# Kernel optimization log

Hardware: AMD Instinct MI355X
Metric: run time of the kernel (lower is better)

Reference implementation:

```python
import jax, jax.numpy as jnp
import numpy as np

B, C, H, W = 8, 256, 64, 64
CQK = C // 8


def setup_inputs() -> dict:
    key = jax.random.key(0)
    ks = jax.random.split(key, 9)
    s_in = 1.0 / np.sqrt(C)
    return {
        "feature1": jax.random.normal(ks[0], (B, C, H, W), jnp.float32),
        "feature2": jax.random.normal(ks[1], (B, C, H, W), jnp.float32),
        "feature3": jax.random.normal(ks[2], (B, C, H, W), jnp.float32),
        # 1x1 conv weights stored as [out_ch, in_ch]
        "wq": jax.random.uniform(ks[3], (CQK, C), jnp.float32, -s_in, s_in),
        "bq": jax.random.uniform(ks[4], (CQK,), jnp.float32, -s_in, s_in),
        "wk": jax.random.uniform(ks[5], (CQK, C), jnp.float32, -s_in, s_in),
        "bk": jax.random.uniform(ks[6], (CQK,), jnp.float32, -s_in, s_in),
        "wv": jax.random.uniform(ks[7], (C, C), jnp.float32, -s_in, s_in),
        "bv": jax.random.uniform(ks[8], (C,), jnp.float32, -s_in, s_in),
    }


def reference(feature1, feature2, feature3, wq, bq, wk, bk, wv, bv):
    b, c, h, w = feature1.shape
    hw = h * w
    # 1x1 convs == per-pixel channel GEMMs
    q = jnp.einsum('bchw,oc->bohw', feature1, wq) + bq[None, :, None, None]
    k = jnp.einsum('bchw,oc->bohw', feature2, wk) + bk[None, :, None, None]
    v = jnp.einsum('bchw,oc->bohw', feature3, wv) + bv[None, :, None, None]
    q = q.reshape(b, -1, hw).transpose(0, 2, 1)  # [b, hw, cqk]
    k = k.reshape(b, -1, hw)                      # [b, cqk, hw]
    v = v.reshape(b, -1, hw)                      # [b, c, hw]
    attn = jax.nn.softmax(jnp.einsum('bnc,bcm->bnm', q, k), axis=-1)  # [b, hw, hw]
    # fused = value @ attn^T  -> [b, c, hw]
    fused = jnp.einsum('bcm,bnm->bcn', v, attn)
    return fused.reshape(b, c, h, w)
```

## Files before the change

kernel.cpp:

```cpp
#include <hip/hip_runtime.h>
#include <math.h>

#define BATCH 8
#define CH    256
#define HWPIX 4096
#define CQK_  32

typedef __bf16 bf16x8 __attribute__((ext_vector_type(8)));
typedef __bf16 bf16x4 __attribute__((ext_vector_type(4)));
typedef __bf16 bf16x2 __attribute__((ext_vector_type(2)));
typedef float  f32x4  __attribute__((ext_vector_type(4)));

#define FS_STR 68

static __device__ inline bf16x8 ld_frag(const __bf16* p) {
  bf16x4 lo = *(const bf16x4*)p;
  bf16x4 hi = *(const bf16x4*)(p + 4);
  return __builtin_shufflevector(lo, hi, 0, 1, 2, 3, 4, 5, 6, 7);
}

static __device__ inline bf16x8 w_frag(const float* p) {
  const float4 a = *(const float4*)p;
  const float4 b = *(const float4*)(p + 4);
  bf16x8 r;
  r[0] = (__bf16)a.x; r[1] = (__bf16)a.y; r[2] = (__bf16)a.z; r[3] = (__bf16)a.w;
  r[4] = (__bf16)b.x; r[5] = (__bf16)b.y; r[6] = (__bf16)b.z; r[7] = (__bf16)b.w;
  return r;
}

__global__ __launch_bounds__(512, 4) void proj_all(
    const float* __restrict__ f1, const float* __restrict__ f2,
    const float* __restrict__ f3,
    const float* __restrict__ wq, const float* __restrict__ bq,
    const float* __restrict__ wk, const float* __restrict__ bk,
    const float* __restrict__ wv, const float* __restrict__ bv,
    __bf16* __restrict__ qT, __bf16* __restrict__ kT, __bf16* __restrict__ vv)
{
  __shared__ __align__(16) __bf16 f_s[2][128 * FS_STR];
  const int t    = threadIdx.x;
  const int w    = __builtin_amdgcn_readfirstlane(t >> 6);
  const int lane = t & 63;
  const int q16  = lane & 15;
  const int quad = lane >> 4;
  const int b    = blockIdx.z;
  const int n0   = blockIdx.x * 128;
  const int mode = blockIdx.y;

  if (mode == 0) {
    const int half = t >> 8;
    const int th   = t & 255;
    const int px   = (th & 31) * 4;
    const int g2   = (th >> 5) * 2;
    const int isK  = w >> 2;
    const int qr   = w & 3;

    const float* fsrc = (half ? f2 : f1) + (size_t)b * CH * HWPIX + n0;
    __bf16* fdst = f_s[half];
    const float* wmat = isK ? wk : wq;

    f32x4 acc[2][2];
#pragma unroll
    for (int i = 0; i < 2; ++i)
#pragma unroll
      for (int j = 0; j < 2; ++j) acc[i][j] = (f32x4){0.f, 0.f, 0.f, 0.f};

    float4 rg_[8];
#define PLOAD(c0)                                                               \
    _Pragma("unroll") for (int cc = 0; cc < 4; ++cc) {                          \
      const int c = (c0) + 16 * cc + g2;                                        \
      rg_[2 * cc]     = *(const float4*)&fsrc[(size_t)c * HWPIX + px];          \
      rg_[2 * cc + 1] = *(const float4*)&fsrc[(size_t)(c + 1) * HWPIX + px];    \
    }
    PLOAD(0);
    for (int c0 = 0; c0 < CH; c0 += 64) {
      __syncthreads();
#pragma unroll
      for (int cc = 0; cc < 4; ++cc) {
        const int c = 16 * cc + g2;
#pragma unroll
        for (int i = 0; i < 4; ++i) {
          bf16x2 pk;
          pk[0] = (__bf16)((const float*)&rg_[2 * cc])[i];
          pk[1] = (__bf16)((const float*)&rg_[2 * cc + 1])[i];
          *(bf16x2*)&fdst[(px + i) * FS_STR + c] = pk;
        }
      }
      __syncthreads();
      if (c0 < CH - 64) PLOAD(c0 + 64);
      bf16x8 af[2][2];
#pragma unroll
      for (int rg = 0; rg < 2; ++rg)
#pragma unroll
        for (int kh = 0; kh < 2; ++kh)
          af[rg][kh] = ld_frag(&f_s[isK][(32 * qr + 16 * rg + q16) * FS_STR
                                         + 32 * kh + quad * 8]);
#pragma unroll
      for (int ot = 0; ot < 2; ++ot)
#pragma unroll
        for (int kh = 0; kh < 2; ++kh) {
          const bf16x8 wf =
              w_frag(wmat + (size_t)(16 * ot + q16) * CH + c0 + 32 * kh + quad * 8);
#pragma unroll
          for (int rg = 0; rg < 2; ++rg)
            acc[ot][rg] = __builtin_amdgcn_mfma_f32_16x16x32_bf16(
                af[rg][kh], wf, acc[ot][rg], 0, 0, 0);
        }
    }
    const float* bias = isK ? bk : bq;
    __bf16* outT = isK ? kT : qT;
    const float b0 = bias[q16], b1 = bias[16 + q16];
#pragma unroll
    for (int rg = 0; rg < 2; ++rg)
#pragma unroll
      for (int r = 0; r < 4; ++r) {
        const size_t row = (size_t)b * HWPIX + n0 + 32 * qr + 16 * rg + quad * 4 + r;
        outT[row * CQK_ + q16]      = (__bf16)(acc[0][rg][r] + b0);
        outT[row * CQK_ + 16 + q16] = (__bf16)(acc[1][rg][r] + b1);
      }
#undef PLOAD
  } else {
    const int px = (t & 31) * 4;
    const int g2 = (t >> 5) * 2;
    const float* f3b = f3 + (size_t)b * CH * HWPIX + n0;

    f32x4 acc[2][8];
#pragma unroll
    for (int ct = 0; ct < 2; ++ct)
#pragma unroll
      for (int nt = 0; nt < 8; ++nt) acc[ct][nt] = (f32x4){0.f, 0.f, 0.f, 0.f};

    float4 r_[4];
#define VLOAD(c0)                                                               \
    _Pragma("unroll") for (int cc = 0; cc < 2; ++cc) {                          \
      const int c = (c0) + 32 * cc + g2;                                        \
      r_[2 * cc]     = *(const float4*)&f3b[(size_t)c * HWPIX + px];            \
      r_[2 * cc + 1] = *(const float4*)&f3b[(size_t)(c + 1) * HWPIX + px];      \
    }
    VLOAD(0);
    for (int c0 = 0; c0 < CH; c0 += 64) {
      __syncthreads();
#pragma unroll
      for (int cc = 0; cc < 2; ++cc) {
        const int c = 32 * cc + g2;
#pragma unroll
        for (int i = 0; i < 4; ++i) {
          bf16x2 pk;
          pk[0] = (__bf16)((const float*)&r_[2 * cc])[i];
          pk[1] = (__bf16)((const float*)&r_[2 * cc + 1])[i];
          *(bf16x2*)&f_s[0][(px + i) * FS_STR + c] = pk;
        }
      }
      __syncthreads();
      if (c0 < CH - 64) VLOAD(c0 + 64);
      bf16x8 af[2][2];
#pragma unroll
      for (int ct = 0; ct < 2; ++ct)
#pragma unroll
        for (int kh = 0; kh < 2; ++kh)
          af[ct][kh] = w_frag(wv + (size_t)(32 * w + 16 * ct + q16) * CH
                              + c0 + 32 * kh + quad * 8);
#pragma unroll
      for (int nt = 0; nt < 8; ++nt) {
#pragma unroll
        for (int kh = 0; kh < 2; ++kh) {
          const bf16x8 bfr =
              ld_frag(&f_s[0][(16 * nt + q16) * FS_STR + 32 * kh + quad * 8]);
#pragma unroll
          for (int ct = 0; ct < 2; ++ct)
            acc[ct][nt] = __builtin_amdgcn_mfma_f32_16x16x32_bf16(
                af[ct][kh], bfr, acc[ct][nt], 0, 0, 0);
        }
      }
    }
#pragma unroll
    for (int ct = 0; ct < 2; ++ct) {
      const float4 bi = *(const float4*)&bv[32 * w + 16 * ct + quad * 4];
#pragma unroll
      for (int nt = 0; nt < 8; ++nt) {
#pragma unroll
        for (int r = 0; r < 4; ++r) {
          const int c = 32 * w + 16 * ct + quad * 4 + r;
          vv[((size_t)b * CH + c) * HWPIX + n0 + 16 * nt + q16] =
              (__bf16)(acc[ct][nt][r] + ((const float*)&bi)[r]);
        }
      }
    }
#undef VLOAD
  }
}

__global__ __launch_bounds__(512, 4) void attn_kernel(
    const __bf16* __restrict__ qT, const __bf16* __restrict__ kT,
    const __bf16* __restrict__ vv, float* __restrict__ out)
{
  __shared__ __align__(16) __bf16 p_s[2][64 * 64];
  __shared__ float L_s[2][64];

  const int t    = threadIdx.x;
  const int w    = __builtin_amdgcn_readfirstlane(t >> 6);
  const int lane = t & 63;
  const int q16  = lane & 15;
  const int quad = lane >> 4;
  const int qb   = w & 3;
  const int hb   = w >> 2;
  const int swz  = (q16 & 7) << 4;

  const int b    = blockIdx.x & 7;
  const int qt   = blockIdx.x >> 3;
  const int q0   = qt * 64;
  const int ioff = qt & 63;

  const __bf16* kTb = kT + (size_t)b * HWPIX * CQK_;
  const size_t koff = (size_t)(32 * hb + q16) * CQK_ + quad * 8;

  const __bf16* vb[2];
#pragma unroll
  for (int ct = 0; ct < 2; ++ct)
    vb[ct] = vv + ((size_t)b * CH + 32 * w + 16 * ct + q16) * HWPIX + quad * 8;

  const bf16x8 qfrag =
      *(const bf16x8*)(qT + ((size_t)b * HWPIX + q0 + 16 * qb + q16) * CQK_ + quad * 8);

  f32x4 oacc[2][4];
#pragma unroll
  for (int i = 0; i < 2; ++i)
#pragma unroll
    for (int j = 0; j < 4; ++j)
      oacc[i][j] = (f32x4){0.f, 0.f, 0.f, 0.f};
  float Lp = 0.f;

  bf16x8 kf[2];
#pragma unroll
  for (int mt = 0; mt < 2; ++mt)
    kf[mt] = *(const bf16x8*)(kTb + (size_t)ioff * (64 * CQK_) + koff + mt * 512);
  {
    f32x4 Sv[2];
#pragma unroll
    for (int mt = 0; mt < 2; ++mt)
      Sv[mt] = __builtin_amdgcn_mfma_f32_16x16x32_bf16(
          kf[mt], qfrag, (f32x4){0.f, 0.f, 0.f, 0.f}, 0, 0, 0);
    const __bf16* kb1 = kTb + (size_t)((ioff + 1) & 63) * (64 * CQK_);
#pragma unroll
    for (int mt = 0; mt < 2; ++mt)
      kf[mt] = *(const bf16x8*)(kb1 + koff + mt * 512);
    char* pw = (char*)p_s[0] + (16 * qb + q16) * 128;
#pragma unroll
    for (int mt = 0; mt < 2; ++mt) {
      bf16x4 pk;
#pragma unroll
      for (int r = 0; r < 4; ++r) {
        const float e = __expf(Sv[mt][r]);
        Lp += e;
        pk[r] = (__bf16)e;
      }
      *(bf16x4*)(pw + ((64 * hb + 32 * mt + 8 * quad) ^ swz)) = pk;
    }
  }
  __syncthreads();

  for (int i = 0; i < 64; ++i) {
    const int jj = (i + ioff) & 63;

    bf16x8 vf[2][2];
#pragma unroll
    for (int ct = 0; ct < 2; ++ct)
#pragma unroll
      for (int mh = 0; mh < 2; ++mh)
        vf[ct][mh] = *(const bf16x8*)(vb[ct] + jj * 64 + mh * 32);

    const char* pb = (const char*)p_s[i & 1];
    bf16x8 pf[4][2];
#pragma unroll
    for (int nt = 0; nt < 4; ++nt)
#pragma unroll
      for (int mh = 0; mh < 2; ++mh)
        pf[nt][mh] = *(const bf16x8*)(pb + (16 * nt + q16) * 128
                                      + ((64 * mh + 16 * quad) ^ swz));

    if (i < 63) {
      f32x4 Sv[2];
#pragma unroll
      for (int mt = 0; mt < 2; ++mt)
        Sv[mt] = __builtin_amdgcn_mfma_f32_16x16x32_bf16(
            kf[mt], qfrag, (f32x4){0.f, 0.f, 0.f, 0.f}, 0, 0, 0);
      const __bf16* kb2 = kTb + (size_t)((i + 2 + ioff) & 63) * (64 * CQK_);
#pragma unroll
      for (int mt = 0; mt < 2; ++mt)
        kf[mt] = *(const bf16x8*)(kb2 + koff + mt * 512);
      char* pw = (char*)p_s[(i + 1) & 1] + (16 * qb + q16) * 128;
#pragma unroll
      for (int mt = 0; mt < 2; ++mt) {
        bf16x4 pk;
#pragma unroll
        for (int r = 0; r < 4; ++r) {
          const float e = __expf(Sv[mt][r]);
          Lp += e;
          pk[r] = (__bf16)e;
        }
        *(bf16x4*)(pw + ((64 * hb + 32 * mt + 8 * quad) ^ swz)) = pk;
      }
    }

#pragma unroll
    for (int ct = 0; ct < 2; ++ct)
#pragma unroll
      for (int nt = 0; nt < 4; ++nt)
#pragma unroll
        for (int mh = 0; mh < 2; ++mh)
          oacc[ct][nt] = __builtin_amdgcn_mfma_f32_16x16x32_bf16(
              vf[ct][mh], pf[nt][mh], oacc[ct][nt], 0, 0, 0);

    __syncthreads();
  }

  Lp += __shfl_xor(Lp, 16);
  Lp += __shfl_xor(Lp, 32);
  if (quad == 0) L_s[hb][16 * qb + q16] = Lp;
  __syncthreads();

  float rinv[4];
#pragma unroll
  for (int nt = 0; nt < 4; ++nt)
    rinv[nt] = 1.0f / (L_s[0][16 * nt + q16] + L_s[1][16 * nt + q16]);

  float* ob = out + ((size_t)b * CH + 32 * w) * HWPIX + q0;
#pragma unroll
  for (int ct = 0; ct < 2; ++ct)
#pragma unroll
    for (int r = 0; r < 4; ++r)
#pragma unroll
      for (int nt = 0; nt < 4; ++nt)
        ob[(size_t)(16 * ct + quad * 4 + r) * HWPIX + 16 * nt + q16] =
            oacc[ct][nt][r] * rinv[nt];
}

extern "C" void kernel_launch(void* const* d_in, const int* in_sizes, int n_in,
                              void* d_out, int out_size, void* d_ws, size_t ws_size,
                              hipStream_t stream)
{
  const float* f1 = (const float*)d_in[0];
  const float* f2 = (const float*)d_in[1];
  const float* f3 = (const float*)d_in[2];
  const float* wq = (const float*)d_in[3];
  const float* bq = (const float*)d_in[4];
  const float* wk = (const float*)d_in[5];
  const float* bk = (const float*)d_in[6];
  const float* wv = (const float*)d_in[7];
  const float* bv = (const float*)d_in[8];
  float* outp = (float*)d_out;

  __bf16* qTw = (__bf16*)d_ws;
  __bf16* kTw = qTw + (size_t)BATCH * HWPIX * CQK_;
  __bf16* vw  = kTw + (size_t)BATCH * HWPIX * CQK_;

  proj_all<<<dim3(32, 2, 8), 512, 0, stream>>>(f1, f2, f3, wq, bq, wk, bk, wv, bv,
                                               qTw, kTw, vw);
  attn_kernel<<<dim3(512), 512, 0, stream>>>(qTw, kTw, vw, outp);
}
```

Before: 293.8 us.

## Warp-specialize attention kernel into score/exp producer and PV MFMA consumer warps

Splits the 8 warps of the attention block into 4 producer warps that compute QK^T scores, exponentials and row sums into shared memory, and 4 consumer warps that run the P·V MFMAs with register double-buffered V loads. Each consumer warp now owns 64 channels instead of 32, so its accumulator tile grows to 4x4. The per-block staggered key-tile start offset is dropped. Launch bounds fall from 4 to 2 blocks per CU to fit the larger register footprint. Barrier counts must match exactly between the two branches, and lower occupancy could reduce latency hiding.

```diff
diff --git a/kernel.cpp b/kernel.cpp
--- a/kernel.cpp
+++ b/kernel.cpp
@@ -189,107 +189,50 @@
   }
 }
 
-__global__ __launch_bounds__(512, 4) void attn_kernel(
+__global__ __launch_bounds__(512, 2) void attn_kernel(
     const __bf16* __restrict__ qT, const __bf16* __restrict__ kT,
     const __bf16* __restrict__ vv, float* __restrict__ out)
 {
   __shared__ __align__(16) __bf16 p_s[2][64 * 64];
-  __shared__ float L_s[2][64];
+  __shared__ float L_s[64];
 
   const int t    = threadIdx.x;
   const int w    = __builtin_amdgcn_readfirstlane(t >> 6);
   const int lane = t & 63;
   const int q16  = lane & 15;
   const int quad = lane >> 4;
-  const int qb   = w & 3;
-  const int hb   = w >> 2;
   const int swz  = (q16 & 7) << 4;
 
-  const int b    = blockIdx.x & 7;
-  const int qt   = blockIdx.x >> 3;
-  const int q0   = qt * 64;
-  const int ioff = qt & 63;
-
-  const __bf16* kTb = kT + (size_t)b * HWPIX * CQK_;
-  const size_t koff = (size_t)(32 * hb + q16) * CQK_ + quad * 8;
-
-  const __bf16* vb[2];
-#pragma unroll
-  for (int ct = 0; ct < 2; ++ct)
-    vb[ct] = vv + ((size_t)b * CH + 32 * w + 16 * ct + q16) * HWPIX + quad * 8;
-
-  const bf16x8 qfrag =
-      *(const bf16x8*)(qT + ((size_t)b * HWPIX + q0 + 16 * qb + q16) * CQK_ + quad * 8);
-
-  f32x4 oacc[2][4];
-#pragma unroll
-  for (int i = 0; i < 2; ++i)
-#pragma unroll
-    for (int j = 0; j < 4; ++j)
-      oacc[i][j] = (f32x4){0.f, 0.f, 0.f, 0.f};
-  float Lp = 0.f;
-
-  bf16x8 kf[2];
-#pragma unroll
-  for (int mt = 0; mt < 2; ++mt)
-    kf[mt] = *(const bf16x8*)(kTb + (size_t)ioff * (64 * CQK_) + koff + mt * 512);
-  {
-    f32x4 Sv[2];
-#pragma unroll
-    for (int mt = 0; mt < 2; ++mt)
-      Sv[mt] = __builtin_amdgcn_mfma_f32_16x16x32_bf16(
-          kf[mt], qfrag, (f32x4){0.f, 0.f, 0.f, 0.f}, 0, 0, 0);
-    const __bf16* kb1 = kTb + (size_t)((ioff + 1) & 63) * (64 * CQK_);
-#pragma unroll
-    for (int mt = 0; mt < 2; ++mt)
-      kf[mt] = *(const bf16x8*)(kb1 + koff + mt * 512);
-    char* pw = (char*)p_s[0] + (16 * qb + q16) * 128;
-#pragma unroll
-    for (int mt = 0; mt < 2; ++mt) {
-      bf16x4 pk;
-#pragma unroll
-      for (int r = 0; r < 4; ++r) {
-        const float e = __expf(Sv[mt][r]);
-        Lp += e;
-        pk[r] = (__bf16)e;
-      }
-      *(bf16x4*)(pw + ((64 * hb + 32 * mt + 8 * quad) ^ swz)) = pk;
-    }
-  }
-  __syncthreads();
-
-  for (int i = 0; i < 64; ++i) {
-    const int jj = (i + ioff) & 63;
-
-    bf16x8 vf[2][2];
-#pragma unroll
-    for (int ct = 0; ct < 2; ++ct)
-#pragma unroll
-      for (int mh = 0; mh < 2; ++mh)
-        vf[ct][mh] = *(const bf16x8*)(vb[ct] + jj * 64 + mh * 32);
-
-    const char* pb = (const char*)p_s[i & 1];
-    bf16x8 pf[4][2];
-#pragma unroll
-    for (int nt = 0; nt < 4; ++nt)
-#pragma unroll
-      for (int mh = 0; mh < 2; ++mh)
-        pf[nt][mh] = *(const bf16x8*)(pb + (16 * nt + q16) * 128
-                                      + ((64 * mh + 16 * quad) ^ swz));
-
-    if (i < 63) {
-      f32x4 Sv[2];
-#pragma unroll
-      for (int mt = 0; mt < 2; ++mt)
+  const int b  = blockIdx.x & 7;
+  const int q0 = (blockIdx.x >> 3) * 64;
+
+  if (w < 4) {
+    const int qb = w;
+    const __bf16* kTb = kT + (size_t)b * HWPIX * CQK_;
+    const size_t koffp = (size_t)q16 * CQK_ + quad * 8;
+
+    const bf16x8 qfrag =
+        *(const bf16x8*)(qT + ((size_t)b * HWPIX + q0 + 16 * qb + q16) * CQK_ + quad * 8);
+
+    float Lp = 0.f;
+    bf16x8 kf[4];
+#pragma unroll
+    for (int mt = 0; mt < 4; ++mt)
+      kf[mt] = *(const bf16x8*)(kTb + mt * 512 + koffp);
+
+    {
+      f32x4 Sv[4];
+#pragma unroll
+      for (int mt = 0; mt < 4; ++mt)
         Sv[mt] = __builtin_amdgcn_mfma_f32_16x16x32_bf16(
             kf[mt], qfrag, (f32x4){0.f, 0.f, 0.f, 0.f}, 0, 0, 0);
-      const __bf16* kb2 = kTb + (size_t)((i + 2 + ioff) & 63) * (64 * CQK_);
-#pragma unroll
-      for (int mt = 0; mt < 2; ++mt)
-        kf[mt] = *(const bf16x8*)(kb2 + koff + mt * 512);
-      char* pw = (char*)p_s[(i + 1) & 1] + (16 * qb + q16) * 128;
-#pragma unroll
-      for (int mt = 0; mt < 2; ++mt) {
+      const __bf16* kb1 = kTb + 2048;
+#pragma unroll
+      for (int mt = 0; mt < 4; ++mt)
+        kf[mt] = *(const bf16x8*)(kb1 + mt * 512 + koffp);
+      char* pw = (char*)p_s[0] + (16 * qb + q16) * 128;
+#pragma unroll
+      for (int mt = 0; mt < 4; ++mt) {
         bf16x4 pk;
 #pragma unroll
         for (int r = 0; r < 4; ++r) {
@@ -297,41 +240,109 @@
           Lp += e;
           pk[r] = (__bf16)e;
         }
-        *(bf16x4*)(pw + ((64 * hb + 32 * mt + 8 * quad) ^ swz)) = pk;
-      }
-    }
-
-#pragma unroll
-    for (int ct = 0; ct < 2; ++ct)
-#pragma unroll
-      for (int nt = 0; nt < 4; ++nt)
-#pragma unroll
-        for (int mh = 0; mh < 2; ++mh)
-          oacc[ct][nt] = __builtin_amdgcn_mfma_f32_16x16x32_bf16(
-              vf[ct][mh], pf[nt][mh], oacc[ct][nt], 0, 0, 0);
-
+        *(bf16x4*)(pw + ((32 * mt + 8 * quad) ^ swz)) = pk;
+      }
+    }
     __syncthreads();
+
+    for (int i = 0; i < 64; ++i) {
+      if (i < 63) {
+        f32x4 Sv[4];
+#pragma unroll
+        for (int mt = 0; mt < 4; ++mt)
+          Sv[mt] = __builtin_amdgcn_mfma_f32_16x16x32_bf16(
+              kf[mt], qfrag, (f32x4){0.f, 0.f, 0.f, 0.f}, 0, 0, 0);
+        const __bf16* kb2 = kTb + (size_t)((i + 2) & 63) * 2048;
+#pragma unroll
+        for (int mt = 0; mt < 4; ++mt)
+          kf[mt] = *(const bf16x8*)(kb2 + mt * 512 + koffp);
+        char* pw = (char*)p_s[(i + 1) & 1] + (16 * qb + q16) * 128;
+#pragma unroll
+        for (int mt = 0; mt < 4; ++mt) {
+          bf16x4 pk;
+#pragma unroll
+          for (int r = 0; r < 4; ++r) {
+            const float e = __expf(Sv[mt][r]);
+            Lp += e;
+            pk[r] = (__bf16)e;
+          }
+          *(bf16x4*)(pw + ((32 * mt + 8 * quad) ^ swz)) = pk;
+        }
+      }
+      __syncthreads();
+    }
+
+    Lp += __shfl_xor(Lp, 16);
+    Lp += __shfl_xor(Lp, 32);
+    if (quad == 0) L_s[16 * qb + q16] = Lp;
+    __syncthreads();
+  } else {
+    const int cc = w - 4;
+    const __bf16* vb[4];
+#pragma unroll
+    for (int ct = 0; ct < 4; ++ct)
+      vb[ct] = vv + ((size_t)b * CH + 64 * cc + 16 * ct + q16) * HWPIX + quad * 8;
+
+    f32x4 oacc[4][4];
+#pragma unroll
+    for (int i = 0; i < 4; ++i)
+#pragma unroll
+      for (int j = 0; j < 4; ++j)
+        oacc[i][j] = (f32x4){0.f, 0.f, 0.f, 0.f};
+
+    bf16x8 vfA[4][2], vfB[4][2];
+#pragma unroll
+    for (int ct = 0; ct < 4; ++ct)
+#pragma unroll
+      for (int mh = 0; mh < 2; ++mh)
+        vfA[ct][mh] = *(const bf16x8*)(vb[ct] + mh * 32);
+    __syncthreads();
+
+#define CITER(I, VCUR, VNXT)                                                    \
+    {                                                                           \
+      const int i_ = (I);                                                       \
+      if (i_ < 63) {     \
+        const size_t vt = (size_t)(i_ + 1) * 64;                                \
+        _Pragma("unroll") for (int ct = 0; ct < 4; ++ct)                        \
+          _Pragma("unroll") for (int mh = 0; mh < 2; ++mh)                      \
+            VNXT[ct][mh] = *(const bf16x8*)(vb[ct] + vt + mh * 32);             \
+      }                                                                         \
+      const char* pb = (const char*)p_s[i_ & 1];                                \
+      _Pragma("unroll") for (int mh = 0; mh < 2; ++mh) {                        \
+        bf16x8 pf[4];                                                           \
+        _Pragma("unroll") for (int nt = 0; nt < 4; ++nt)                        \
+          pf[nt] = *(const bf16x8*)(pb + (16 * nt + q16) * 128                  \
+                                    + ((64 * mh + 16 * quad) ^ swz));           \
+        _Pragma("unroll") for (int ct = 0; ct < 4; ++ct)                        \
+          _Pragma("unroll") for (int nt = 0; nt < 4; ++nt)                      \
+            oacc[ct][nt] = __builtin_amdgcn_mfma_f32_16x16x32_bf16(             \
+                VCUR[ct][mh], pf[nt], oacc[ct][nt], 0, 0, 0);                   \
+      }                                                                         \
+      __syncthreads();                                                          \
+    }
+
+    for (int i = 0; i < 64; i += 2) {
+      CITER(i, vfA, vfB);
+      CITER(i + 1, vfB, vfA);
+    }
+#undef CITER
+
+    __syncthreads();
+
+    float rinv[4];
+#pragma unroll
+    for (int nt = 0; nt < 4; ++nt) rinv[nt] = 1.0f / L_s[16 * nt + q16];
+
+    float* ob = out + ((size_t)b * CH + 64 * cc) * HWPIX + q0;
+#pragma unroll
+    for (int ct = 0; ct < 4; ++ct)
+#pragma unroll
+      for (int r = 0; r < 4; ++r)
+#pragma unroll
+        for (int nt = 0; nt < 4; ++nt)
+          ob[(size_t)(16 * ct + quad * 4 + r) * HWPIX + 16 * nt + q16] =
+              oacc[ct][nt][r] * rinv[nt];
   }
-
-  Lp += __shfl_xor(Lp, 16);
-  Lp += __shfl_xor(Lp, 32);
-  if (quad == 0) L_s[hb][16 * qb + q16] = Lp;
-  __syncthreads();
-
-  float rinv[4];
-#pragma unroll
-  for (int nt = 0; nt < 4; ++nt)
-    rinv[nt] = 1.0f / (L_s[0][16 * nt + q16] + L_s[1][16 * nt + q16]);
-
-  float* ob = out + ((size_t)b * CH + 32 * w) * HWPIX + q0;
-#pragma unroll
-  for (int ct = 0; ct < 2; ++ct)
-#pragma unroll
-    for (int r = 0; r < 4; ++r)
-#pragma unroll
-      for (int nt = 0; nt < 4; ++nt)
-        ob[(size_t)(16 * ct + quad * 4 + r) * HWPIX + 16 * nt + q16] =
-            oacc[ct][nt][r] * rinv[nt];
 }
 
 extern "C" void kernel_launch(void* const* d_in, const int* in_sizes, int n_in,
```

Result: slower. 317.5 us (+8.0%).
